# Kernel tuning notes

Measured on AMD Instinct MI355X. Metric: run time of the kernel, lower is better.

The kernel has to match this reference:

```python
import jax, jax.numpy as jnp
import numpy as np

B, S, D = 2, 2048, 2048
H, DH = 16, 128
FF = 5632  # multiple_of-rounded 2/3 * 4 * D
EPS = 1e-6


def rmsnorm(x, w):
    x32 = x.astype(jnp.float32)
    n = x32 * jax.lax.rsqrt(jnp.mean(x32 * x32, axis=-1, keepdims=True) + EPS)
    return n.astype(x.dtype) * w


def apply_rope(x, cos, sin):
    # x: [B,S,H,DH]; cos/sin: [S,DH//2]
    xr = x[..., 0::2].astype(jnp.float32)
    xi = x[..., 1::2].astype(jnp.float32)
    c = cos[None, :, None, :]
    s = sin[None, :, None, :]
    or_ = xr * c - xi * s
    oi_ = xr * s + xi * c
    out = jnp.stack([or_, oi_], axis=-1).reshape(x.shape)
    return out.astype(x.dtype)


def setup_inputs() -> dict:
    key = jax.random.key(0)
    ks = jax.random.split(key, 12)
    t = jnp.arange(S, dtype=jnp.float32)
    inv = 1.0 / (10000.0 ** (jnp.arange(0, DH, 2, dtype=jnp.float32) / DH))
    ang = t[:, None] * inv[None, :]
    sc = 0.02
    return {
        "hidden_states": jax.random.normal(ks[0], (B, S, D), jnp.float32),
        "freqs_cos": jnp.cos(ang),
        "freqs_sin": jnp.sin(ang),
        "wq": jax.random.normal(ks[1], (D, H * DH), jnp.float32) * sc,
        "wk": jax.random.normal(ks[2], (D, H * DH), jnp.float32) * sc,
        "wv": jax.random.normal(ks[3], (D, H * DH), jnp.float32) * sc,
        "wo": jax.random.normal(ks[4], (H * DH, D), jnp.float32) * sc,
        "w1": jax.random.normal(ks[5], (D, FF), jnp.float32) * sc,
        "w2": jax.random.normal(ks[6], (FF, D), jnp.float32) * sc,
        "w3": jax.random.normal(ks[7], (D, FF), jnp.float32) * sc,
        "attn_norm_w": jnp.ones((D,), jnp.float32),
        "ffn_norm_w": jnp.ones((D,), jnp.float32),
    }


def reference(hidden_states, freqs_cos, freqs_sin, wq, wk, wv, wo, w1, w2, w3,
              attn_norm_w, ffn_norm_w):
    x = rmsnorm(hidden_states, attn_norm_w)
    q = (x @ wq).reshape(B, S, H, DH)
    k = (x @ wk).reshape(B, S, H, DH)
    v = (x @ wv).reshape(B, S, H, DH)
    q = apply_rope(q, freqs_cos, freqs_sin)
    k = apply_rope(k, freqs_cos, freqs_sin)
    # scores: [B,H,Sq,Sk]
    scores = jnp.einsum("bqhd,bkhd->bhqk", q, k) / jnp.sqrt(jnp.float32(DH))
    causal = jnp.triu(jnp.full((S, S), -jnp.inf, jnp.float32), k=1)
    scores = scores + causal[None, None]
    probs = jax.nn.softmax(scores.astype(jnp.float32), axis=-1).astype(q.dtype)
    attn = jnp.einsum("bhqk,bkhd->bqhd", probs, v).reshape(B, S, H * DH)
    h = hidden_states + attn @ wo
    y = rmsnorm(h, ffn_norm_w)
    ff = (jax.nn.silu(y @ w1) * (y @ w3)) @ w2
    return h + ff
```

## Files before the change

kernel.cpp:

```cpp
#include <hip/hip_runtime.h>

#define B_ 2
#define S_ 2048
#define D_ 2048
#define H_ 16
#define DH_ 128
#define FF_ 5632
#define M_ (B_*S_)

typedef unsigned short u16;
typedef unsigned int u32;
typedef __attribute__((ext_vector_type(8))) short short8;
typedef __attribute__((ext_vector_type(4))) float floatx4;

__device__ __forceinline__ float bf2f(u16 h) {
  union { u32 u; float f; } v; v.u = ((u32)h) << 16; return v.f;
}
__device__ __forceinline__ u16 f2bf(float f) {
  union { float f; u32 u; } v; v.f = f;
  u32 u = v.u;
  return (u16)((u + 0x7FFFu + ((u >> 16) & 1u)) >> 16);
}
__device__ __forceinline__ bool probe_f32(const u32* p) { return (p[0] & 0xFFFFu) == 0u; }

__global__ __launch_bounds__(256) void rmsnorm_kernel(
    const void* __restrict__ x, const void* __restrict__ w, u16* __restrict__ o,
    const u32* __restrict__ probe, int x_ext) {
  const bool m = probe_f32(probe);
  const bool xf = m && (x_ext != 0);
  const int row = blockIdx.x;
  const int tid = threadIdx.x;
  float v[8];
  if (xf) {
    const float* xr = (const float*)x + (size_t)row * D_;
    float4 p0 = *(const float4*)(xr + tid * 8);
    float4 p1 = *(const float4*)(xr + tid * 8 + 4);
    v[0]=p0.x; v[1]=p0.y; v[2]=p0.z; v[3]=p0.w;
    v[4]=p1.x; v[5]=p1.y; v[6]=p1.z; v[7]=p1.w;
  } else {
    const u16* xr = (const u16*)x + (size_t)row * D_;
    uint4 p = *(const uint4*)(xr + tid * 8);
    u32 ua[4] = {p.x, p.y, p.z, p.w};
#pragma unroll
    for (int i = 0; i < 4; ++i) {
      v[2*i]   = bf2f((u16)(ua[i] & 0xffffu));
      v[2*i+1] = bf2f((u16)(ua[i] >> 16));
    }
  }
  float ss = 0.f;
#pragma unroll
  for (int i = 0; i < 8; ++i) ss += v[i] * v[i];
#pragma unroll
  for (int d = 1; d < 64; d <<= 1) ss += __shfl_xor(ss, d);
  __shared__ float sbuf[4];
  if ((tid & 63) == 0) sbuf[tid >> 6] = ss;
  __syncthreads();
  float tot = sbuf[0] + sbuf[1] + sbuf[2] + sbuf[3];
  float sc = rsqrtf(tot * (1.0f / (float)D_) + 1e-6f);
  float wv[8];
  if (m) {
    const float* wr = (const float*)w;
    float4 p0 = *(const float4*)(wr + tid * 8);
    float4 p1 = *(const float4*)(wr + tid * 8 + 4);
    wv[0]=p0.x; wv[1]=p0.y; wv[2]=p0.z; wv[3]=p0.w;
    wv[4]=p1.x; wv[5]=p1.y; wv[6]=p1.z; wv[7]=p1.w;
  } else {
    uint4 pw = *(const uint4*)((const u16*)w + tid * 8);
    u32 uw[4] = {pw.x, pw.y, pw.z, pw.w};
#pragma unroll
    for (int i = 0; i < 4; ++i) {
      wv[2*i]   = bf2f((u16)(uw[i] & 0xffffu));
      wv[2*i+1] = bf2f((u16)(uw[i] >> 16));
    }
  }
  u32 ow[4];
#pragma unroll
  for (int i = 0; i < 4; ++i) {
    float n0 = v[2*i] * sc, n1 = v[2*i+1] * sc;
    if (!m) { n0 = bf2f(f2bf(n0)); n1 = bf2f(f2bf(n1)); }
    n0 *= wv[2*i]; n1 *= wv[2*i+1];
    ow[i] = (u32)f2bf(n0) | ((u32)f2bf(n1) << 16);
  }
  uint4 po; po.x = ow[0]; po.y = ow[1]; po.z = ow[2]; po.w = ow[3];
  *(uint4*)(o + (size_t)row * D_ + tid * 8) = po;
}

template<int EPI>
__global__ __launch_bounds__(256, 2) void gemm_kernel(
    const u16* __restrict__ A, const void* __restrict__ Bm,
    void* C, const void* Res,
    int Ndim, int Kdim, const u32* __restrict__ probe, int res_ext, int c_ext) {
  const bool m = probe_f32(probe);
  const bool rf = m && (res_ext != 0);
  const bool cf = m && (c_ext != 0);
  __shared__ u16 As[128][40];
  __shared__ u16 Bs[128][40];
  const int tid = threadIdx.x;
  const int wave = tid >> 6, lane = tid & 63;
  const int quad = lane >> 4, l16 = lane & 15;
  const int waveM = wave & 1, waveN = wave >> 1;
  const int mb = blockIdx.y * 128, nb = blockIdx.x * 128;

  floatx4 acc[4][4];
#pragma unroll
  for (int i = 0; i < 4; ++i)
#pragma unroll
    for (int j = 0; j < 4; ++j) { floatx4 z = {0.f,0.f,0.f,0.f}; acc[i][j] = z; }

  const int kTiles = Kdim >> 5;
  for (int kt = 0; kt < kTiles; ++kt) {
    const int k0 = kt << 5;
#pragma unroll
    for (int i = 0; i < 2; ++i) {
      int c = tid + i * 256;
      int row = c >> 2, kc = (c & 3) << 3;
      uint4 val = *(const uint4*)(A + (size_t)(mb + row) * Kdim + k0 + kc);
      *(uint4*)&As[row][kc] = val;
    }
    {
      int n = tid & 127, kh = tid >> 7;
      u16 t[16];
      if (m) {
        const float* Bf = (const float*)Bm;
#pragma unroll
        for (int j = 0; j < 16; ++j)
          t[j] = f2bf(Bf[(size_t)(k0 + kh * 16 + j) * Ndim + nb + n]);
      } else {
        const u16* Bh = (const u16*)Bm;
#pragma unroll
        for (int j = 0; j < 16; ++j)
          t[j] = Bh[(size_t)(k0 + kh * 16 + j) * Ndim + nb + n];
      }
      uint4 w0, w1;
      w0.x = (u32)t[0] | ((u32)t[1] << 16);   w0.y = (u32)t[2] | ((u32)t[3] << 16);
      w0.z = (u32)t[4] | ((u32)t[5] << 16);   w0.w = (u32)t[6] | ((u32)t[7] << 16);
      w1.x = (u32)t[8] | ((u32)t[9] << 16);   w1.y = (u32)t[10] | ((u32)t[11] << 16);
      w1.z = (u32)t[12] | ((u32)t[13] << 16); w1.w = (u32)t[14] | ((u32)t[15] << 16);
      *(uint4*)&Bs[n][kh * 16]     = w0;
      *(uint4*)&Bs[n][kh * 16 + 8] = w1;
    }
    __syncthreads();
    short8 af[4], bfr[4];
#pragma unroll
    for (int i = 0; i < 4; ++i)
      af[i] = *(const short8*)&As[waveM * 64 + i * 16 + l16][quad * 8];
#pragma unroll
    for (int i = 0; i < 4; ++i)
      bfr[i] = *(const short8*)&Bs[waveN * 64 + i * 16 + l16][quad * 8];
#pragma unroll
    for (int mi = 0; mi < 4; ++mi)
#pragma unroll
      for (int ni = 0; ni < 4; ++ni)
        acc[mi][ni] = __builtin_amdgcn_mfma_f32_16x16x32_bf16(af[mi], bfr[ni], acc[mi][ni], 0, 0, 0);
    __syncthreads();
  }
#pragma unroll
  for (int mi = 0; mi < 4; ++mi)
#pragma unroll
    for (int ni = 0; ni < 4; ++ni) {
      int gm0 = mb + waveM * 64 + mi * 16 + quad * 4;
      int gn  = nb + waveN * 64 + ni * 16 + l16;
#pragma unroll
      for (int r = 0; r < 4; ++r) {
        float v = acc[mi][ni][r];
        size_t idx = (size_t)(gm0 + r) * Ndim + gn;
        if (EPI == 1) v += rf ? ((const float*)Res)[idx] : bf2f(((const u16*)Res)[idx]);
        if (EPI == 2) v = v / (1.f + __expf(-v));
        if (EPI == 3) v *= bf2f(((const u16*)Res)[idx]);
        if (cf) ((float*)C)[idx] = v;
        else    ((u16*)C)[idx] = f2bf(v);
      }
    }
}

__global__ __launch_bounds__(256) void rope_kernel(
    u16* __restrict__ q, u16* __restrict__ k,
    const void* __restrict__ ct, const void* __restrict__ st,
    const u32* __restrict__ probe) {
  const bool m = probe_f32(probe);
  int idx = blockIdx.x * 256 + threadIdx.x;
  int row = idx >> 10;
  int rem = idx & 1023;
  int h = rem >> 6, j = rem & 63;
  int s = row & (S_ - 1);
  size_t a = (size_t)row * D_ + h * DH_ + 2 * j;
  float c, sn;
  if (m) { c = ((const float*)ct)[s * 64 + j]; sn = ((const float*)st)[s * 64 + j]; }
  else   { c = bf2f(((const u16*)ct)[s * 64 + j]); sn = bf2f(((const u16*)st)[s * 64 + j]); }
  u32 qq = *(u32*)(q + a);
  float xr = bf2f((u16)(qq & 0xffffu)), xi = bf2f((u16)(qq >> 16));
  *(u32*)(q + a) = (u32)f2bf(xr * c - xi * sn) | ((u32)f2bf(xr * sn + xi * c) << 16);
  u32 kk = *(u32*)(k + a);
  xr = bf2f((u16)(kk & 0xffffu)); xi = bf2f((u16)(kk >> 16));
  *(u32*)(k + a) = (u32)f2bf(xr * c - xi * sn) | ((u32)f2bf(xr * sn + xi * c) << 16);
}

__global__ __launch_bounds__(256) void vtrans_kernel(
    const u16* __restrict__ v, u16* __restrict__ vt) {
  __shared__ u16 tl[64][72];
  int s0 = blockIdx.x * 64, d0 = blockIdx.y * 64;
  int bh = blockIdx.z, b = bh >> 4, h = bh & 15;
  int tid = threadIdx.x;
#pragma unroll
  for (int i = 0; i < 2; ++i) {
    int c = tid + i * 256;
    int row = c >> 3, dc = (c & 7) << 3;
    uint4 val = *(const uint4*)(v + (size_t)(b * S_ + s0 + row) * D_ + h * DH_ + d0 + dc);
    *(uint4*)&tl[row][dc] = val;
  }
  __syncthreads();
#pragma unroll
  for (int i = 0; i < 2; ++i) {
    int c = tid + i * 256;
    int dr = c >> 3, sc = (c & 7) << 3;
    u16 t[8];
#pragma unroll
    for (int j = 0; j < 8; ++j) t[j] = tl[sc + j][dr];
    uint4 w0;
    w0.x = (u32)t[0] | ((u32)t[1] << 16); w0.y = (u32)t[2] | ((u32)t[3] << 16);
    w0.z = (u32)t[4] | ((u32)t[5] << 16); w0.w = (u32)t[6] | ((u32)t[7] << 16);
    *(uint4*)(vt + (size_t)(bh * DH_ + d0 + dr) * S_ + s0 + sc) = w0;
  }
}

__global__ __launch_bounds__(256, 1) void attn_kernel(
    const u16* __restrict__ q, const u16* __restrict__ k,
    const u16* __restrict__ vt, u16* __restrict__ o) {
  __shared__ u16 Ks[64][136];
  __shared__ u16 Vs[128][72];
  __shared__ u16 Ps[4][32][72];
  const int qt = blockIdx.x, bh = blockIdx.y;
  const int b = bh >> 4, h = bh & 15;
  const int tid = threadIdx.x;
  const int wave = tid >> 6, lane = tid & 63;
  const int quad = lane >> 4, l16 = lane & 15;

  short8 qa[2][4];
  const u16* qbase = q + (size_t)(b * S_ + qt * 128 + wave * 32) * D_ + h * DH_;
#pragma unroll
  for (int mi = 0; mi < 2; ++mi)
#pragma unroll
    for (int ks = 0; ks < 4; ++ks)
      qa[mi][ks] = *(const short8*)(qbase + (size_t)(mi * 16 + l16) * D_ + ks * 32 + quad * 8);

  float m_i[2][4], l_i[2][4];
  floatx4 acc_o[2][8];
#pragma unroll
  for (int mi = 0; mi < 2; ++mi) {
#pragma unroll
    for (int r = 0; r < 4; ++r) { m_i[mi][r] = -1e30f; l_i[mi][r] = 0.f; }
#pragma unroll
    for (int nd = 0; nd < 8; ++nd) { floatx4 z = {0.f,0.f,0.f,0.f}; acc_o[mi][nd] = z; }
  }

  const int nkt = 2 * qt + 2;
  for (int kt = 0; kt < nkt; ++kt) {
#pragma unroll
    for (int i = 0; i < 4; ++i) {
      int c = tid + i * 256;
      int row = c >> 4, dc = (c & 15) << 3;
      uint4 val = *(const uint4*)(k + (size_t)(b * S_ + kt * 64 + row) * D_ + h * DH_ + dc);
      *(uint4*)&Ks[row][dc] = val;
    }
#pragma unroll
    for (int i = 0; i < 4; ++i) {
      int c = tid + i * 256;
      int row = c >> 3, sc = (c & 7) << 3;
      uint4 val = *(const uint4*)(vt + (size_t)(bh * DH_ + row) * S_ + kt * 64 + sc);
      *(uint4*)&Vs[row][sc] = val;
    }
    __syncthreads();

    floatx4 accs[2][4];
#pragma unroll
    for (int mi = 0; mi < 2; ++mi)
#pragma unroll
      for (int ni = 0; ni < 4; ++ni) { floatx4 z = {0.f,0.f,0.f,0.f}; accs[mi][ni] = z; }
#pragma unroll
    for (int ks = 0; ks < 4; ++ks) {
      short8 kf[4];
#pragma unroll
      for (int ni = 0; ni < 4; ++ni)
        kf[ni] = *(const short8*)&Ks[ni * 16 + l16][ks * 32 + quad * 8];
#pragma unroll
      for (int mi = 0; mi < 2; ++mi)
#pragma unroll
        for (int ni = 0; ni < 4; ++ni)
          accs[mi][ni] = __builtin_amdgcn_mfma_f32_16x16x32_bf16(qa[mi][ks], kf[ni], accs[mi][ni], 0, 0, 0);
    }

    const float scl = 0.08838834764831845f;
    const bool diag = (kt >= 2 * qt);
#pragma unroll
    for (int mi = 0; mi < 2; ++mi) {
#pragma unroll
      for (int r = 0; r < 4; ++r) {
        int qg = qt * 128 + wave * 32 + mi * 16 + quad * 4 + r;
        float mx = -1e30f;
#pragma unroll
        for (int ni = 0; ni < 4; ++ni) {
          float sv = accs[mi][ni][r] * scl;
          int kg = kt * 64 + ni * 16 + l16;
          if (diag && kg > qg) sv = -1e30f;
          accs[mi][ni][r] = sv;
          mx = fmaxf(mx, sv);
        }
#pragma unroll
        for (int d = 1; d < 16; d <<= 1) mx = fmaxf(mx, __shfl_xor(mx, d));
        float mn = fmaxf(m_i[mi][r], mx);
        float al = __expf(m_i[mi][r] - mn);
        float rs = 0.f;
#pragma unroll
        for (int ni = 0; ni < 4; ++ni) {
          float p = __expf(accs[mi][ni][r] - mn);
          accs[mi][ni][r] = p;
          rs += p;
        }
#pragma unroll
        for (int d = 1; d < 16; d <<= 1) rs += __shfl_xor(rs, d);
        l_i[mi][r] = l_i[mi][r] * al + rs;
        m_i[mi][r] = mn;
#pragma unroll
        for (int nd = 0; nd < 8; ++nd) acc_o[mi][nd][r] *= al;
      }
    }
#pragma unroll
    for (int mi = 0; mi < 2; ++mi)
#pragma unroll
      for (int ni = 0; ni < 4; ++ni)
#pragma unroll
        for (int r = 0; r < 4; ++r)
          Ps[wave][mi * 16 + quad * 4 + r][ni * 16 + l16] = f2bf(accs[mi][ni][r]);
    __syncthreads();
#pragma unroll
    for (int kss = 0; kss < 2; ++kss) {
      short8 vf[8], pf[2];
#pragma unroll
      for (int nd = 0; nd < 8; ++nd)
        vf[nd] = *(const short8*)&Vs[nd * 16 + l16][kss * 32 + quad * 8];
#pragma unroll
      for (int mi = 0; mi < 2; ++mi)
        pf[mi] = *(const short8*)&Ps[wave][mi * 16 + l16][kss * 32 + quad * 8];
#pragma unroll
      for (int mi = 0; mi < 2; ++mi)
#pragma unroll
        for (int nd = 0; nd < 8; ++nd)
          acc_o[mi][nd] = __builtin_amdgcn_mfma_f32_16x16x32_bf16(pf[mi], vf[nd], acc_o[mi][nd], 0, 0, 0);
    }
    __syncthreads();
  }
#pragma unroll
  for (int mi = 0; mi < 2; ++mi)
#pragma unroll
    for (int r = 0; r < 4; ++r) {
      float inv = 1.0f / l_i[mi][r];
      int row = b * S_ + qt * 128 + wave * 32 + mi * 16 + quad * 4 + r;
#pragma unroll
      for (int nd = 0; nd < 8; ++nd)
        o[(size_t)row * D_ + h * DH_ + nd * 16 + l16] = f2bf(acc_o[mi][nd][r] * inv);
    }
}

extern "C" void kernel_launch(void* const* d_in, const int* in_sizes, int n_in,
                              void* d_out, int out_size, void* d_ws, size_t ws_size,
                              hipStream_t stream) {
  const void* hidden = d_in[0];
  const void* fcos   = d_in[1];
  const void* fsin   = d_in[2];
  const void* wq     = d_in[3];
  const void* wk     = d_in[4];
  const void* wv     = d_in[5];
  const void* wo     = d_in[6];
  const void* w1     = d_in[7];
  const void* w2     = d_in[8];
  const void* w3     = d_in[9];
  const void* anw    = d_in[10];
  const void* fnw    = d_in[11];
  const u32* probe = (const u32*)fcos;
  u16* ws  = (u16*)d_ws;

  const size_t SB = (size_t)M_ * D_;
  u16* qb = ws;
  u16* vb = ws + SB;
  u16* xb = ws + 2 * SB;
  u16* kb = ws + 3 * SB;
  u16* t1 = ws + 2 * SB;
  u16* vtb = (u16*)d_out;

  dim3 gD(D_ / 128, M_ / 128);
  dim3 gF(FF_ / 128, M_ / 128);

  rmsnorm_kernel<<<M_, 256, 0, stream>>>(hidden, anw, xb, probe, 1);
  gemm_kernel<0><<<gD, 256, 0, stream>>>(xb, wq, qb, nullptr, D_, D_, probe, 0, 0);
  gemm_kernel<0><<<gD, 256, 0, stream>>>(xb, wk, kb, nullptr, D_, D_, probe, 0, 0);
  gemm_kernel<0><<<gD, 256, 0, stream>>>(xb, wv, vb, nullptr, D_, D_, probe, 0, 0);
  rope_kernel<<<(M_ * H_ * 64) / 256, 256, 0, stream>>>(qb, kb, fcos, fsin, probe);
  vtrans_kernel<<<dim3(S_ / 64, DH_ / 64, B_ * H_), 256, 0, stream>>>(vb, vtb);
  attn_kernel<<<dim3(S_ / 128, B_ * H_), 256, 0, stream>>>(qb, kb, vtb, xb);
  gemm_kernel<1><<<gD, 256, 0, stream>>>(xb, wo, vb, hidden, D_, D_, probe, 1, 0);
  rmsnorm_kernel<<<M_, 256, 0, stream>>>(vb, fnw, qb, probe, 0);
  gemm_kernel<2><<<gF, 256, 0, stream>>>(qb, w1, t1, nullptr, FF_, D_, probe, 0, 0);
  gemm_kernel<3><<<gF, 256, 0, stream>>>(qb, w3, t1, t1, FF_, D_, probe, 0, 0);
  gemm_kernel<1><<<gD, 256, 0, stream>>>(t1, w2, d_out, vb, D_, FF_, probe, 0, 1);
}
```

Before: 1.414 ms.

## Pre-transpose weights to bf16 and use direct global-to-LDS GEMM

Measured after the change: 1.202 ms. 15.0% less time.

```diff
diff --git a/kernel.cpp b/kernel.cpp
--- a/kernel.cpp
+++ b/kernel.cpp
@@ -22,6 +22,11 @@
   return (u16)((u + 0x7FFFu + ((u >> 16) & 1u)) >> 16);
 }
 __device__ __forceinline__ bool probe_f32(const u32* p) { return (p[0] & 0xFFFFu) == 0u; }
+
+__device__ __forceinline__ void gl_lds16(const void* g, void* l) {
+  __builtin_amdgcn_global_load_lds((const __attribute__((address_space(1))) void*)g,
+                                   (__attribute__((address_space(3))) void*)l, 16, 0, 0);
+}
 
 __global__ __launch_bounds__(256) void rmsnorm_kernel(
     const void* __restrict__ x, const void* __restrict__ w, u16* __restrict__ o,
@@ -83,6 +88,104 @@
   }
   uint4 po; po.x = ow[0]; po.y = ow[1]; po.z = ow[2]; po.w = ow[3];
   *(uint4*)(o + (size_t)row * D_ + tid * 8) = po;
+}
+
+__global__ __launch_bounds__(256) void wtrans_kernel(
+    const float* __restrict__ W, u16* __restrict__ WT, int Kdim, int Ndim) {
+  __shared__ u16 tl[64][72];
+  const int n0 = blockIdx.x * 64, k0 = blockIdx.y * 64;
+  const int tid = threadIdx.x;
+#pragma unroll
+  for (int i = 0; i < 4; ++i) {
+    int c = tid + i * 256;
+    int kr = c >> 4, nc = (c & 15) * 4;
+    float4 v = *(const float4*)(W + (size_t)(k0 + kr) * Ndim + n0 + nc);
+    uint2 p;
+    p.x = (u32)f2bf(v.x) | ((u32)f2bf(v.y) << 16);
+    p.y = (u32)f2bf(v.z) | ((u32)f2bf(v.w) << 16);
+    *(uint2*)&tl[kr][nc] = p;
+  }
+  __syncthreads();
+#pragma unroll
+  for (int i = 0; i < 2; ++i) {
+    int c = tid + i * 256;
+    int nr = c >> 3, kc = (c & 7) * 8;
+    u16 t[8];
+#pragma unroll
+    for (int j = 0; j < 8; ++j) t[j] = tl[kc + j][nr];
+    uint4 w0;
+    w0.x = (u32)t[0] | ((u32)t[1] << 16); w0.y = (u32)t[2] | ((u32)t[3] << 16);
+    w0.z = (u32)t[4] | ((u32)t[5] << 16); w0.w = (u32)t[6] | ((u32)t[7] << 16);
+    *(uint4*)(WT + (size_t)(n0 + nr) * Kdim + k0 + kc) = w0;
+  }
+}
+
+template<int EPI>
+__global__ __launch_bounds__(256) void gemm_bt_kernel(
+    const u16* __restrict__ A, const u16* __restrict__ BT,
+    void* C, const void* Res, int Ndim, int Kdim, int res_f32, int c_f32) {
+  __shared__ u16 As[128 * 32];
+  __shared__ u16 Bs[128 * 32];
+  const int tid = threadIdx.x;
+  const int wave = tid >> 6, lane = tid & 63;
+  const int quad = lane >> 4, l16 = lane & 15;
+  const int waveM = wave & 1, waveN = wave >> 1;
+  const int mb = blockIdx.y * 128, nb = blockIdx.x * 128;
+
+  const int srow = wave * 32 + (lane >> 2);
+  const int skof = (lane & 3) * 8;
+  const u16* aP0 = A  + (size_t)(mb + srow) * Kdim + skof;
+  const u16* aP1 = aP0 + (size_t)16 * Kdim;
+  const u16* bP0 = BT + (size_t)(nb + srow) * Kdim + skof;
+  const u16* bP1 = bP0 + (size_t)16 * Kdim;
+  u16* lA0 = As + (wave * 2)     * 512;
+  u16* lA1 = As + (wave * 2 + 1) * 512;
+  u16* lB0 = Bs + (wave * 2)     * 512;
+  u16* lB1 = Bs + (wave * 2 + 1) * 512;
+
+  floatx4 acc[4][4];
+#pragma unroll
+  for (int i = 0; i < 4; ++i)
+#pragma unroll
+    for (int j = 0; j < 4; ++j) { floatx4 z = {0.f,0.f,0.f,0.f}; acc[i][j] = z; }
+
+  const int kTiles = Kdim >> 5;
+  for (int kt = 0; kt < kTiles; ++kt) {
+    gl_lds16(aP0, lA0); gl_lds16(aP1, lA1);
+    gl_lds16(bP0, lB0); gl_lds16(bP1, lB1);
+    aP0 += 32; aP1 += 32; bP0 += 32; bP1 += 32;
+    __syncthreads();
+    short8 af[4], bfr[4];
+#pragma unroll
+    for (int i = 0; i < 4; ++i)
+      af[i] = *(const short8*)&As[(size_t)(waveM * 64 + i * 16 + l16) * 32 + quad * 8];
+#pragma unroll
+    for (int i = 0; i < 4; ++i)
+      bfr[i] = *(const short8*)&Bs[(size_t)(waveN * 64 + i * 16 + l16) * 32 + quad * 8];
+#pragma unroll
+    for (int mi = 0; mi < 4; ++mi)
+#pragma unroll
+      for (int ni = 0; ni < 4; ++ni)
+        acc[mi][ni] = __builtin_amdgcn_mfma_f32_16x16x32_bf16(af[mi], bfr[ni], acc[mi][ni], 0, 0, 0);
+    __syncthreads();
+  }
+#pragma unroll
+  for (int mi = 0; mi < 4; ++mi)
+#pragma unroll
+    for (int ni = 0; ni < 4; ++ni) {
+      int gm0 = mb + waveM * 64 + mi * 16 + quad * 4;
+      int gn  = nb + waveN * 64 + ni * 16 + l16;
+#pragma unroll
+      for (int r = 0; r < 4; ++r) {
+        float v = acc[mi][ni][r];
+        size_t idx = (size_t)(gm0 + r) * Ndim + gn;
+        if (EPI == 1) v += res_f32 ? ((const float*)Res)[idx] : bf2f(((const u16*)Res)[idx]);
+        if (EPI == 2) v = v / (1.f + __expf(-v));
+        if (EPI == 3) v *= bf2f(((const u16*)Res)[idx]);
+        if (c_f32) ((float*)C)[idx] = v;
+        else       ((u16*)C)[idx] = f2bf(v);
+      }
+    }
 }
 
 template<int EPI>
@@ -380,6 +483,9 @@
   u16* ws  = (u16*)d_ws;
 
   const size_t SB = (size_t)M_ * D_;
+  const size_t FB = (size_t)M_ * FF_;
+  const size_t DD = (size_t)D_ * D_;
+  const size_t DF = (size_t)D_ * FF_;
   u16* qb = ws;
   u16* vb = ws + SB;
   u16* xb = ws + 2 * SB;
@@ -387,19 +493,53 @@
   u16* t1 = ws + 2 * SB;
   u16* vtb = (u16*)d_out;
 
+  const size_t baseElems = 2 * SB + FB;
+  const size_t wElems = 4 * DD + 3 * DF;
+  const bool fast = ws_size >= (baseElems + wElems) * sizeof(u16);
+
   dim3 gD(D_ / 128, M_ / 128);
   dim3 gF(FF_ / 128, M_ / 128);
 
-  rmsnorm_kernel<<<M_, 256, 0, stream>>>(hidden, anw, xb, probe, 1);
-  gemm_kernel<0><<<gD, 256, 0, stream>>>(xb, wq, qb, nullptr, D_, D_, probe, 0, 0);
-  gemm_kernel<0><<<gD, 256, 0, stream>>>(xb, wk, kb, nullptr, D_, D_, probe, 0, 0);
-  gemm_kernel<0><<<gD, 256, 0, stream>>>(xb, wv, vb, nullptr, D_, D_, probe, 0, 0);
-  rope_kernel<<<(M_ * H_ * 64) / 256, 256, 0, stream>>>(qb, kb, fcos, fsin, probe);
-  vtrans_kernel<<<dim3(S_ / 64, DH_ / 64, B_ * H_), 256, 0, stream>>>(vb, vtb);
-  attn_kernel<<<dim3(S_ / 128, B_ * H_), 256, 0, stream>>>(qb, kb, vtb, xb);
-  gemm_kernel<1><<<gD, 256, 0, stream>>>(xb, wo, vb, hidden, D_, D_, probe, 1, 0);
-  rmsnorm_kernel<<<M_, 256, 0, stream>>>(vb, fnw, qb, probe, 0);
-  gemm_kernel<2><<<gF, 256, 0, stream>>>(qb, w1, t1, nullptr, FF_, D_, probe, 0, 0);
-  gemm_kernel<3><<<gF, 256, 0, stream>>>(qb, w3, t1, t1, FF_, D_, probe, 0, 0);
-  gemm_kernel<1><<<gD, 256, 0, stream>>>(t1, w2, d_out, vb, D_, FF_, probe, 0, 1);
-}
+  if (fast) {
+    u16* wqT = ws + baseElems;
+    u16* wkT = wqT + DD;
+    u16* wvT = wkT + DD;
+    u16* woT = wvT + DD;
+    u16* w1T = woT + DD;
+    u16* w3T = w1T + DF;
+    u16* w2T = w3T + DF;
+    wtrans_kernel<<<dim3(D_/64,  D_/64),  256, 0, stream>>>((const float*)wq, wqT, D_, D_);
+    wtrans_kernel<<<dim3(D_/64,  D_/64),  256, 0, stream>>>((const float*)wk, wkT, D_, D_);
+    wtrans_kernel<<<dim3(D_/64,  D_/64),  256, 0, stream>>>((const float*)wv, wvT, D_, D_);
+    wtrans_kernel<<<dim3(D_/64,  D_/64),  256, 0, stream>>>((const float*)wo, woT, D_, D_);
+    wtrans_kernel<<<dim3(FF_/64, D_/64),  256, 0, stream>>>((const float*)w1, w1T, D_, FF_);
+    wtrans_kernel<<<dim3(FF_/64, D_/64),  256, 0, stream>>>((const float*)w3, w3T, D_, FF_);
+    wtrans_kernel<<<dim3(D_/64,  FF_/64), 256, 0, stream>>>((const float*)w2, w2T, FF_, D_);
+
+    rmsnorm_kernel<<<M_, 256, 0, stream>>>(hidden, anw, xb, probe, 1);
+    gemm_bt_kernel<0><<<gD, 256, 0, stream>>>(xb, wqT, qb, nullptr, D_, D_, 0, 0);
+    gemm_bt_kernel<0><<<gD, 256, 0, stream>>>(xb, wkT, kb, nullptr, D_, D_, 0, 0);
+    gemm_bt_kernel<0><<<gD, 256, 0, stream>>>(xb, wvT, vb, nullptr, D_, D_, 0, 0);
+    rope_kernel<<<(M_ * H_ * 64) / 256, 256, 0, stream>>>(qb, kb, fcos, fsin, probe);
+    vtrans_kernel<<<dim3(S_ / 64, DH_ / 64, B_ * H_), 256, 0, stream>>>(vb, vtb);
+    attn_kernel<<<dim3(S_ / 128, B_ * H_), 256, 0, stream>>>(qb, kb, vtb, xb);
+    gemm_bt_kernel<1><<<gD, 256, 0, stream>>>(xb, woT, vb, hidden, D_, D_, 1, 0);
+    rmsnorm_kernel<<<M_, 256, 0, stream>>>(vb, fnw, qb, probe, 0);
+    gemm_bt_kernel<2><<<gF, 256, 0, stream>>>(qb, w1T, t1, nullptr, FF_, D_, 0, 0);
+    gemm_bt_kernel<3><<<gF, 256, 0, stream>>>(qb, w3T, t1, t1, FF_, D_, 0, 0);
+    gemm_bt_kernel<1><<<gD, 256, 0, stream>>>(t1, w2T, d_out, vb, D_, FF_, 0, 1);
+  } else {
+    rmsnorm_kernel<<<M_, 256, 0, stream>>>(hidden, anw, xb, probe, 1);
+    gemm_kernel<0><<<gD, 256, 0, stream>>>(xb, wq, qb, nullptr, D_, D_, probe, 0, 0);
+    gemm_kernel<0><<<gD, 256, 0, stream>>>(xb, wk, kb, nullptr, D_, D_, probe, 0, 0);
+    gemm_kernel<0><<<gD, 256, 0, stream>>>(xb, wv, vb, nullptr, D_, D_, probe, 0, 0);
+    rope_kernel<<<(M_ * H_ * 64) / 256, 256, 0, stream>>>(qb, kb, fcos, fsin, probe);
+    vtrans_kernel<<<dim3(S_ / 64, DH_ / 64, B_ * H_), 256, 0, stream>>>(vb, vtb);
+    attn_kernel<<<dim3(S_ / 128, B_ * H_), 256, 0, stream>>>(qb, kb, vtb, xb);
+    gemm_kernel<1><<<gD, 256, 0, stream>>>(xb, wo, vb, hidden, D_, D_, probe, 1, 0);
+    rmsnorm_kernel<<<M_, 256, 0, stream>>>(vb, fnw, qb, probe, 0);
+    gemm_kernel<2><<<gF, 256, 0, stream>>>(qb, w1, t1, nullptr, FF_, D_, probe, 0, 0);
+    gemm_kernel<3><<<gF, 256, 0, stream>>>(qb, w3, t1, t1, FF_, D_, probe, 0, 0);
+    gemm_kernel<1><<<gD, 256, 0, stream>>>(t1, w2, d_out, vb, D_, FF_, probe, 0, 1);
+  }
+}
```
